# Performance work log

Measured on AMD Instinct MI355X. Metric: run time of the kernel, lower is better.

## Reference

```python
import jax, jax.numpy as jnp
import numpy as np


def setup_inputs() -> dict:
    key = jax.random.key(0)
    ks = jax.random.split(key, 8)
    N, DIN, DOUT = 8192, 1024, 1024
    s = 1.0 / np.sqrt(DIN)
    return {
        "gAB": jax.random.normal(ks[0], (N, DIN), dtype=jnp.float32),
        "gAG": jax.random.normal(ks[1], (N, DIN), dtype=jnp.float32),
        "Wab": jax.random.normal(ks[2], (DIN, DOUT), dtype=jnp.float32) * s,
        "Wag": jax.random.normal(ks[3], (DIN, DOUT), dtype=jnp.float32) * s,
        "bab": jax.random.normal(ks[4], (DOUT,), dtype=jnp.float32) * 0.01,
        "bag": jax.random.normal(ks[5], (DOUT,), dtype=jnp.float32) * 0.01,
        "sAB": jax.random.normal(ks[6], (N, DOUT), dtype=jnp.float32),
        "sAG": jax.random.normal(ks[7], (N, DOUT), dtype=jnp.float32),
    }


def reference(gAB, gAG, Wab, Wag, bab, bag, sAB, sAG) -> jnp.ndarray:
    # project() per encoder (Linear): [N, DIN] @ [DIN, DOUT] + b
    pAB = gAB @ Wab + bab  # [N, DOUT]
    pAG = gAG @ Wag + bag  # [N, DOUT]
    # torch.diag(pAB @ pAG.T) == row-wise dot product (avoids O(N^2 d) waste)
    h1 = jnp.sum(pAB * pAG, axis=1, keepdims=True)  # [N, 1]
    h2 = jnp.sum(sAB * sAG, axis=1, keepdims=True)  # [N, 1]
    # mean over concatenated (h1, h2) columns, keepdim=True
    h = jnp.mean(jnp.concatenate([h1, h2], axis=1), axis=1, keepdims=True)  # [N, 1]
    return h
```

## Files before the change

### kernel.cpp

```cpp
#include <hip/hip_runtime.h>
#include <hip/hip_bf16.h>
#include <stdint.h>

typedef __attribute__((ext_vector_type(8))) short bf16x8;
typedef __attribute__((ext_vector_type(4))) float f32x4;

#define DIN 1024
#define NROWS 8192

__device__ __forceinline__ unsigned short f2bf(float f) {
    union { float f; unsigned u; } v; v.f = f;
    unsigned r = v.u + 0x7FFFu + ((v.u >> 16) & 1u);
    return (unsigned short)(r >> 16);
}

__device__ __forceinline__ int fswz(int r) { return (r ^ (r >> 2)) & 3; }

__device__ __forceinline__ size_t swz8_byte(int R, int c) {
    return ((size_t)R * DIN + (size_t)(c & ~63)) * 2
         + (size_t)(((((c >> 3) & 7) ^ (R & 7)) << 4))
         + (size_t)((c & 7) * 2);
}

__device__ __forceinline__ void gload_lds16(const void* g, void* l) {
    __builtin_amdgcn_global_load_lds(
        (const __attribute__((address_space(1))) unsigned*)g,
        (__attribute__((address_space(3))) unsigned*)l, 16, 0, 0);
}

__global__ __launch_bounds__(256) void prep_kernel(const float* __restrict__ Wab,
                                                   const float* __restrict__ Wag,
                                                   const float* __restrict__ bab,
                                                   const float* __restrict__ bag,
                                                   float* __restrict__ ws_f,
                                                   unsigned short* __restrict__ Whab,
                                                   unsigned short* __restrict__ Whag) {
    int b = blockIdx.x;
    int wave = threadIdx.x >> 6, lane = threadIdx.x & 63;
    if (b == 256) {
        if (wave == 0) {
            float acc = 0.f;
            for (int j = lane; j < DIN; j += 64) acc += bab[j] * bag[j];
            for (int off = 32; off; off >>= 1) acc += __shfl_xor(acc, off);
            if (lane == 0) ws_f[2048] = acc;
        }
        return;
    }
    int r = b * 4 + wave;
    int fr = fswz(r);
    {
        const float* wrow = Wab + (size_t)r * DIN;
        char* hrow = (char*)Whab + (size_t)r * DIN * 2;
        float acc = 0.f;
#pragma unroll
        for (int it = 0; it < 4; ++it) {
            int col = it * 256 + lane * 4;
            float4 w = *reinterpret_cast<const float4*>(wrow + col);
            float4 bv = *reinterpret_cast<const float4*>(bag + col);
            acc += w.x * bv.x + w.y * bv.y + w.z * bv.z + w.w * bv.w;
            ushort4 h; h.x = f2bf(w.x); h.y = f2bf(w.y); h.z = f2bf(w.z); h.w = f2bf(w.w);
            *reinterpret_cast<ushort4*>(hrow + (col & ~31) * 2 + ((((col >> 3) & 3) ^ fr) << 4) + (col & 7) * 2) = h;
        }
        for (int off = 32; off; off >>= 1) acc += __shfl_xor(acc, off);
        if (lane == 0) ws_f[r] = acc;
    }
    {
        const float* wrow = Wag + (size_t)r * DIN;
        char* hrow = (char*)Whag + (size_t)r * DIN * 2;
        float acc = 0.f;
#pragma unroll
        for (int it = 0; it < 4; ++it) {
            int col = it * 256 + lane * 4;
            float4 w = *reinterpret_cast<const float4*>(wrow + col);
            float4 bv = *reinterpret_cast<const float4*>(bab + col);
            acc += w.x * bv.x + w.y * bv.y + w.z * bv.z + w.w * bv.w;
            ushort4 h; h.x = f2bf(w.x); h.y = f2bf(w.y); h.z = f2bf(w.z); h.w = f2bf(w.w);
            *reinterpret_cast<ushort4*>(hrow + (col & ~31) * 2 + ((((col >> 3) & 3) ^ fr) << 4) + (col & 7) * 2) = h;
        }
        for (int off = 32; off; off >>= 1) acc += __shfl_xor(acc, off);
        if (lane == 0) ws_f[1024 + r] = acc;
    }
}

__global__ __launch_bounds__(512) void mt_kernel(const unsigned short* __restrict__ Whag,
                                                 const unsigned short* __restrict__ Whab,
                                                 unsigned short* __restrict__ Mt) {
    __shared__ unsigned short sm[2][2][2][2048];
    int tid = threadIdx.x;
    int wave = tid >> 6, grp = wave >> 2, w4 = wave & 3;
    int lane = tid & 63, kg = lane >> 4, cl = lane & 15;
    int wr = w4 >> 1, wc = w4 & 1;
    int br = blockIdx.x >> 4, bc = blockIdx.x & 15;
    int u = tid & 255, urow = u >> 2, uchunk = u & 3;

    const char* Abase = (const char*)Whag + ((size_t)(br * 64 + urow) * DIN + grp * 512) * 2 + uchunk * 16;
    const char* Bbase = (const char*)Whab + ((size_t)(bc * 64 + urow) * DIN + grp * 512) * 2 + uchunk * 16;

    int offA[2], offB[2];
#pragma unroll
    for (int m = 0; m < 2; ++m) { int row = wr * 32 + m * 16 + cl; offA[m] = row * 32 + ((kg ^ fswz(row)) << 3); }
#pragma unroll
    for (int n = 0; n < 2; ++n) { int row = wc * 32 + n * 16 + cl; offB[n] = row * 32 + ((kg ^ fswz(row)) << 3); }

    f32x4 acc[2][2] = {};
    gload_lds16(Abase, &sm[grp][0][0][u * 8]);
    gload_lds16(Bbase, &sm[grp][0][1][u * 8]);
    for (int t = 0; t < 16; ++t) {
        int p = t & 1;
        __syncthreads();
        if (t < 15) {
            gload_lds16(Abase + (t + 1) * 64, &sm[grp][p ^ 1][0][u * 8]);
            gload_lds16(Bbase + (t + 1) * 64, &sm[grp][p ^ 1][1][u * 8]);
        }
        bf16x8 af[2], bfr[2];
#pragma unroll
        for (int m = 0; m < 2; ++m) af[m] = *reinterpret_cast<const bf16x8*>(&sm[grp][p][0][offA[m]]);
#pragma unroll
        for (int n = 0; n < 2; ++n) bfr[n] = *reinterpret_cast<const bf16x8*>(&sm[grp][p][1][offB[n]]);
        __builtin_amdgcn_s_setprio(1);
#pragma unroll
        for (int m = 0; m < 2; ++m)
#pragma unroll
            for (int n = 0; n < 2; ++n)
                acc[m][n] = __builtin_amdgcn_mfma_f32_16x16x32_bf16(af[m], bfr[n], acc[m][n], 0, 0, 0);
        __builtin_amdgcn_s_setprio(0);
    }
    __syncthreads();
    float* red = (float*)sm;
    if (grp == 1) {
#pragma unroll
        for (int m = 0; m < 2; ++m)
#pragma unroll
            for (int n = 0; n < 2; ++n)
#pragma unroll
                for (int j = 0; j < 4; ++j)
                    red[(wr * 32 + m * 16 + kg * 4 + j) * 68 + wc * 32 + n * 16 + cl] = acc[m][n][j];
    }
    __syncthreads();
    if (grp == 0) {
#pragma unroll
        for (int m = 0; m < 2; ++m)
#pragma unroll
            for (int n = 0; n < 2; ++n)
#pragma unroll
                for (int j = 0; j < 4; ++j) {
                    int rl = wr * 32 + m * 16 + kg * 4 + j, cll = wc * 32 + n * 16 + cl;
                    float v = acc[m][n][j] + red[rl * 68 + cll];
                    int R = br * 64 + rl, C = bc * 64 + cll;
                    *(unsigned short*)((char*)Mt + swz8_byte(R, C)) = f2bf(v);
                }
    }
}

__global__ __launch_bounds__(256) void stream_kernel(const float* __restrict__ gAB,
                                                     const float* __restrict__ sAB,
                                                     const float* __restrict__ sAG,
                                                     const float* __restrict__ ws_f,
                                                     unsigned short* __restrict__ gABh,
                                                     float* __restrict__ out,
                                                     int writecast) {
    int wave = threadIdx.x >> 6, lane = threadIdx.x & 63;
    int row = blockIdx.x * 4 + wave;
    const float* ga = gAB + (size_t)row * DIN;
    const float* sa = sAB + (size_t)row * DIN;
    const float* sg = sAG + (size_t)row * DIN;
    char* gh = (char*)gABh + (size_t)row * DIN * 2;
    int fr8 = row & 7;
    float acc = 0.f;
#pragma unroll
    for (int cc = 0; cc < 4; ++cc) {
        int col = cc * 256 + lane * 4;
        float4 a = *reinterpret_cast<const float4*>(ga + col);
        float4 x = *reinterpret_cast<const float4*>(sa + col);
        float4 y = *reinterpret_cast<const float4*>(sg + col);
        float4 v = *reinterpret_cast<const float4*>(ws_f + col);
        acc += x.x * y.x + x.y * y.y + x.z * y.z + x.w * y.w;
        acc += a.x * v.x + a.y * v.y + a.z * v.z + a.w * v.w;
        if (writecast) {
            ushort4 h; h.x = f2bf(a.x); h.y = f2bf(a.y); h.z = f2bf(a.z); h.w = f2bf(a.w);
            *reinterpret_cast<ushort4*>(gh + (col & ~63) * 2 + ((((col >> 3) & 7) ^ fr8) << 4) + (col & 7) * 2) = h;
        }
    }
#pragma unroll
    for (int off = 32; off; off >>= 1) acc += __shfl_xor(acc, off);
    if (lane == 0) out[row] = 0.5f * (acc + ws_f[2048]);
}

template <int PRECAST>
__global__ __launch_bounds__(512, 2) void gemm256(const float* __restrict__ gAB,
                                                  const unsigned short* __restrict__ gABh,
                                                  const float* __restrict__ gAG,
                                                  const unsigned short* __restrict__ Mt,
                                                  const float* __restrict__ ws_f,
                                                  float* __restrict__ out) {
    __shared__ unsigned short lds_a[2][256 * 64];
    __shared__ unsigned short lds_b[2][256 * 64];
    constexpr int KSPLIT = 2, KLEN = DIN / KSPLIT, NSTEP = KLEN / 64;
    int b = blockIdx.x;
    int x = b & 7, s = b >> 3;
    int rblk = x + 8 * (s & 3);
    int rem = s >> 2;
    int ks = rem & 1;
    int cblk = rem >> 1;
    int tid = threadIdx.x, wave = tid >> 6, lane = tid & 63;
    int wr = wave >> 2, wc = wave & 3;
    int kg = lane >> 4, cl = lane & 15;
    int row0 = rblk * 256, col0 = cblk * 256;

    const char* Ab = (const char*)gABh + (size_t)row0 * DIN * 2 + (size_t)(ks * KLEN) * 2;
    const char* Bb = (const char*)Mt + (size_t)col0 * DIN * 2 + (size_t)(ks * KLEN) * 2;
    const float* Af = gAB + (size_t)row0 * DIN + ks * KLEN;

    f32x4 acc[8][4] = {};

#define STAGE_B(buf, t)                                                                   \
    _Pragma("unroll")                                                                     \
    for (int it = 0; it < 4; ++it) {                                                      \
        int u = tid + it * 512;                                                           \
        gload_lds16(Bb + (size_t)(u >> 3) * (DIN * 2) + (u & 7) * 16 + (t) * 128,         \
                    (char*)&lds_b[buf][0] + u * 16);                                      \
    }
#define STAGE_A_PRE(buf, t)                                                               \
    _Pragma("unroll")                                                                     \
    for (int it = 0; it < 4; ++it) {                                                      \
        int u = tid + it * 512;                                                           \
        gload_lds16(Ab + (size_t)(u >> 3) * (DIN * 2) + (u & 7) * 16 + (t) * 128,         \
                    (char*)&lds_a[buf][0] + u * 16);                                      \
    }
#define STAGE_A_F32(buf, t)                                                               \
    _Pragma("unroll")                                                                     \
    for (int it = 0; it < 8; ++it) {                                                      \
        int u = tid + it * 512;                                              \
        int row = u >> 4, c4 = u & 15;                          \
        float4 w = *reinterpret_cast<const float4*>(Af + (size_t)row * DIN + (t) * 64 + c4 * 4); \
        ushort4 h; h.x = f2bf(w.x); h.y = f2bf(w.y); h.z = f2bf(w.z); h.w = f2bf(w.w);    \
        *reinterpret_cast<ushort4*>((char*)&lds_a[buf][0] + row * 128 +                   \
                                    (((c4 >> 1) ^ (row & 7)) << 4) + (c4 & 1) * 8) = h;   \
    }

    if (PRECAST) { STAGE_A_PRE(0, 0); } else { STAGE_A_F32(0, 0); }
    STAGE_B(0, 0);

    for (int t = 0; t < NSTEP; ++t) {
        int p = t & 1;
        __syncthreads();
        if (t < NSTEP - 1) {
            if (PRECAST) { STAGE_A_PRE(p ^ 1, t + 1); } else { STAGE_A_F32(p ^ 1, t + 1); }
            STAGE_B(p ^ 1, t + 1);
        }
#pragma unroll
        for (int kk = 0; kk < 2; ++kk) {
            bf16x8 bfr[4];
#pragma unroll
            for (int n = 0; n < 4; ++n) {
                int row = wc * 64 + n * 16 + cl;
                bfr[n] = *reinterpret_cast<const bf16x8*>(&lds_b[p][row * 64 + ((((kk << 2) | kg) ^ (row & 7)) << 3)]);
            }
            bf16x8 af[8];
#pragma unroll
            for (int m = 0; m < 8; ++m) {
                int row = wr * 128 + m * 16 + cl;
                af[m] = *reinterpret_cast<const bf16x8*>(&lds_a[p][row * 64 + ((((kk << 2) | kg) ^ (row & 7)) << 3)]);
            }
            __builtin_amdgcn_s_setprio(1);
#pragma unroll
            for (int m = 0; m < 8; ++m)
#pragma unroll
                for (int n = 0; n < 4; ++n)
                    acc[m][n] = __builtin_amdgcn_mfma_f32_16x16x32_bf16(af[m], bfr[n], acc[m][n], 0, 0, 0);
            __builtin_amdgcn_s_setprio(0);
        }
    }

    const float* vag = ws_f + 1024;
#pragma unroll
    for (int m = 0; m < 8; ++m)
#pragma unroll
        for (int j = 0; j < 4; ++j) {
            int row = row0 + wr * 128 + m * 16 + kg * 4 + j;
            const float* gr = gAG + (size_t)row * DIN;
            float t = 0.f;
#pragma unroll
            for (int n = 0; n < 4; ++n) {
                int col = col0 + wc * 64 + n * 16 + cl;
                float addv = (ks == 0) ? vag[col] : 0.f;
                t += gr[col] * (acc[m][n][j] + addv);
            }
            t += __shfl_xor(t, 1);
            t += __shfl_xor(t, 2);
            t += __shfl_xor(t, 4);
            t += __shfl_xor(t, 8);
            if (cl == 0) atomicAdd(out + row, 0.5f * t);
        }
#undef STAGE_B
#undef STAGE_A_PRE
#undef STAGE_A_F32
}

extern "C" void kernel_launch(void* const* d_in, const int* in_sizes, int n_in,
                              void* d_out, int out_size, void* d_ws, size_t ws_size,
                              hipStream_t stream) {
    const float* gAB = (const float*)d_in[0];
    const float* gAG = (const float*)d_in[1];
    const float* Wab = (const float*)d_in[2];
    const float* Wag = (const float*)d_in[3];
    const float* bab = (const float*)d_in[4];
    const float* bag = (const float*)d_in[5];
    const float* sAB = (const float*)d_in[6];
    const float* sAG = (const float*)d_in[7];
    float* out = (float*)d_out;

    float* ws_f = (float*)d_ws;
    char* base = (char*)d_ws + 16384;
    unsigned short* Mt = (unsigned short*)base;
    unsigned short* Whag = (unsigned short*)(base + (size_t)2 * 1024 * 1024);
    unsigned short* Whab = (unsigned short*)(base + (size_t)4 * 1024 * 1024);
    unsigned short* gABh = (unsigned short*)(base + (size_t)6 * 1024 * 1024);
    size_t need_full = 16384 + (size_t)22 * 1024 * 1024;
    int precast = (ws_size >= need_full) ? 1 : 0;

    prep_kernel<<<257, 256, 0, stream>>>(Wab, Wag, bab, bag, ws_f, Whab, Whag);
    mt_kernel<<<256, 512, 0, stream>>>(Whag, Whab, Mt);
    stream_kernel<<<2048, 256, 0, stream>>>(gAB, sAB, sAG, ws_f, gABh, out, precast);
    if (precast)
        gemm256<1><<<256, 512, 0, stream>>>(gAB, gABh, gAG, Mt, ws_f, out);
    else
        gemm256<0><<<256, 512, 0, stream>>>(gAB, gABh, gAG, Mt, ws_f, out);
}
```

Measured before the change: 71.64 us.

## Triple-buffer GEMM with BK=32 stages and explicit vmcnt waits, add fallback GEMM

Replaces the double-buffered 256x256 GEMM (K-step 64) with a three-stage pipeline using K-step 32 tiles. Loads are issued two steps ahead, and a single barrier per step is guarded by explicit s_waitcnt vmcnt counts instead of __syncthreads. LDS swizzle offsets are precomputed once per thread. The non-precast path gets a separate 128x128 kernel with register-staged fp32 loads. The aim is to hide global-to-LDS latency better. In exchange it halves MFMA work per barrier and lowers the occupancy hint to one block per CU.

New measurement: 78.01 us. +8.9%, slower.

```diff
diff --git a/kernel.cpp b/kernel.cpp
--- a/kernel.cpp
+++ b/kernel.cpp
@@ -186,16 +186,14 @@
     if (lane == 0) out[row] = 0.5f * (acc + ws_f[2048]);
 }
 
-template <int PRECAST>
-__global__ __launch_bounds__(512, 2) void gemm256(const float* __restrict__ gAB,
-                                                  const unsigned short* __restrict__ gABh,
-                                                  const float* __restrict__ gAG,
-                                                  const unsigned short* __restrict__ Mt,
-                                                  const float* __restrict__ ws_f,
-                                                  float* __restrict__ out) {
-    __shared__ unsigned short lds_a[2][256 * 64];
-    __shared__ unsigned short lds_b[2][256 * 64];
-    constexpr int KSPLIT = 2, KLEN = DIN / KSPLIT, NSTEP = KLEN / 64;
+__global__ __launch_bounds__(512, 1) void gemm_pipe(const unsigned short* __restrict__ gABh,
+                                                    const float* __restrict__ gAG,
+                                                    const unsigned short* __restrict__ Mt,
+                                                    const float* __restrict__ ws_f,
+                                                    float* __restrict__ out) {
+    __shared__ unsigned short lds_a[3][256 * 32];
+    __shared__ unsigned short lds_b[3][256 * 32];
+    constexpr int KLEN = 512, NSTEP = 16;
     int b = blockIdx.x;
     int x = b & 7, s = b >> 3;
     int rblk = x + 8 * (s & 3);
@@ -207,70 +205,71 @@
     int kg = lane >> 4, cl = lane & 15;
     int row0 = rblk * 256, col0 = cblk * 256;
 
-    const char* Ab = (const char*)gABh + (size_t)row0 * DIN * 2 + (size_t)(ks * KLEN) * 2;
-    const char* Bb = (const char*)Mt + (size_t)col0 * DIN * 2 + (size_t)(ks * KLEN) * 2;
-    const float* Af = gAB + (size_t)row0 * DIN + ks * KLEN;
+    const char* Ab = (const char*)gABh + (size_t)row0 * (DIN * 2) + (size_t)ks * KLEN * 2;
+    const char* Bb = (const char*)Mt + (size_t)col0 * (DIN * 2) + (size_t)ks * KLEN * 2;
+
+    int offA[8], offB[4];
+#pragma unroll
+    for (int m = 0; m < 8; ++m) { int row = wr * 128 + m * 16 + cl; offA[m] = row * 64 + ((kg ^ (row & 3)) << 4); }
+#pragma unroll
+    for (int n = 0; n < 4; ++n) { int row = wc * 64 + n * 16 + cl; offB[n] = row * 64 + ((kg ^ (row & 3)) << 4); }
+
+#define STAGE(buf, t) do {                                                          \
+    _Pragma("unroll")                                                               \
+    for (int it = 0; it < 2; ++it) {                                                \
+        int u = tid + it * 512;                                                     \
+        int row_ = u >> 2, s_ = u & 3;                                              \
+        int pg = ((((t) & 1) << 2) ^ (row_ & 4)) | s_;                              \
+        gload_lds16(Ab + (size_t)row_ * 2048 + ((t) >> 1) * 128 + pg * 16,          \
+                    (char*)&lds_a[buf][0] + u * 16);                                \
+    }                                                                               \
+    _Pragma("unroll")                                                               \
+    for (int it = 0; it < 2; ++it) {                                                \
+        int u = tid + it * 512;                                                     \
+        int row_ = u >> 2, s_ = u & 3;                                              \
+        int pg = ((((t) & 1) << 2) ^ (row_ & 4)) | s_;                              \
+        gload_lds16(Bb + (size_t)row_ * 2048 + ((t) >> 1) * 128 + pg * 16,          \
+                    (char*)&lds_b[buf][0] + u * 16);                                \
+    }                                                                               \
+} while (0)
 
     f32x4 acc[8][4] = {};
 
-#define STAGE_B(buf, t)                                                                   \
-    _Pragma("unroll")                                                                     \
-    for (int it = 0; it < 4; ++it) {                                                      \
-        int u = tid + it * 512;                                                           \
-        gload_lds16(Bb + (size_t)(u >> 3) * (DIN * 2) + (u & 7) * 16 + (t) * 128,         \
-                    (char*)&lds_b[buf][0] + u * 16);                                      \
-    }
-#define STAGE_A_PRE(buf, t)                                                               \
-    _Pragma("unroll")                                                                     \
-    for (int it = 0; it < 4; ++it) {                                                      \
-        int u = tid + it * 512;                                                           \
-        gload_lds16(Ab + (size_t)(u >> 3) * (DIN * 2) + (u & 7) * 16 + (t) * 128,         \
-                    (char*)&lds_a[buf][0] + u * 16);                                      \
-    }
-#define STAGE_A_F32(buf, t)                                                               \
-    _Pragma("unroll")                                                                     \
-    for (int it = 0; it < 8; ++it) {                                                      \
-        int u = tid + it * 512;                                              \
-        int row = u >> 4, c4 = u & 15;                          \
-        float4 w = *reinterpret_cast<const float4*>(Af + (size_t)row * DIN + (t) * 64 + c4 * 4); \
-        ushort4 h; h.x = f2bf(w.x); h.y = f2bf(w.y); h.z = f2bf(w.z); h.w = f2bf(w.w);    \
-        *reinterpret_cast<ushort4*>((char*)&lds_a[buf][0] + row * 128 +                   \
-                                    (((c4 >> 1) ^ (row & 7)) << 4) + (c4 & 1) * 8) = h;   \
-    }
-
-    if (PRECAST) { STAGE_A_PRE(0, 0); } else { STAGE_A_F32(0, 0); }
-    STAGE_B(0, 0);
+    STAGE(0, 0);
+    STAGE(1, 1);
+    asm volatile("s_waitcnt vmcnt(4)" ::: "memory");
+    __builtin_amdgcn_sched_barrier(0);
+    __builtin_amdgcn_s_barrier();
+    __builtin_amdgcn_sched_barrier(0);
 
     for (int t = 0; t < NSTEP; ++t) {
-        int p = t & 1;
-        __syncthreads();
-        if (t < NSTEP - 1) {
-            if (PRECAST) { STAGE_A_PRE(p ^ 1, t + 1); } else { STAGE_A_F32(p ^ 1, t + 1); }
-            STAGE_B(p ^ 1, t + 1);
-        }
-#pragma unroll
-        for (int kk = 0; kk < 2; ++kk) {
-            bf16x8 bfr[4];
-#pragma unroll
-            for (int n = 0; n < 4; ++n) {
-                int row = wc * 64 + n * 16 + cl;
-                bfr[n] = *reinterpret_cast<const bf16x8*>(&lds_b[p][row * 64 + ((((kk << 2) | kg) ^ (row & 7)) << 3)]);
-            }
-            bf16x8 af[8];
-#pragma unroll
-            for (int m = 0; m < 8; ++m) {
-                int row = wr * 128 + m * 16 + cl;
-                af[m] = *reinterpret_cast<const bf16x8*>(&lds_a[p][row * 64 + ((((kk << 2) | kg) ^ (row & 7)) << 3)]);
-            }
-            __builtin_amdgcn_s_setprio(1);
-#pragma unroll
-            for (int m = 0; m < 8; ++m)
-#pragma unroll
-                for (int n = 0; n < 4; ++n)
-                    acc[m][n] = __builtin_amdgcn_mfma_f32_16x16x32_bf16(af[m], bfr[n], acc[m][n], 0, 0, 0);
-            __builtin_amdgcn_s_setprio(0);
-        }
-    }
+        int cur = t % 3;
+        if (t < NSTEP - 2) {
+            int nxt = (t + 2) % 3;
+            STAGE(nxt, t + 2);
+        }
+        bf16x8 af[8], bfr[4];
+#pragma unroll
+        for (int n = 0; n < 4; ++n) bfr[n] = *reinterpret_cast<const bf16x8*>((char*)&lds_b[cur][0] + offB[n]);
+#pragma unroll
+        for (int m = 0; m < 8; ++m) af[m] = *reinterpret_cast<const bf16x8*>((char*)&lds_a[cur][0] + offA[m]);
+        __builtin_amdgcn_s_setprio(1);
+#pragma unroll
+        for (int m = 0; m < 8; ++m)
+#pragma unroll
+            for (int n = 0; n < 4; ++n)
+                acc[m][n] = __builtin_amdgcn_mfma_f32_16x16x32_bf16(af[m], bfr[n], acc[m][n], 0, 0, 0);
+        __builtin_amdgcn_s_setprio(0);
+        if (t < NSTEP - 2) {
+            asm volatile("s_waitcnt vmcnt(4)" ::: "memory");
+        } else {
+            asm volatile("s_waitcnt vmcnt(0)" ::: "memory");
+        }
+        __builtin_amdgcn_sched_barrier(0);
+        __builtin_amdgcn_s_barrier();
+        __builtin_amdgcn_sched_barrier(0);
+    }
+#undef STAGE
 
     const float* vag = ws_f + 1024;
 #pragma unroll
@@ -292,9 +291,99 @@
             t += __shfl_xor(t, 8);
             if (cl == 0) atomicAdd(out + row, 0.5f * t);
         }
-#undef STAGE_B
-#undef STAGE_A_PRE
-#undef STAGE_A_F32
+}
+
+__global__ __launch_bounds__(256, 4) void gemm_fb(const float* __restrict__ gAB,
+                                                  const float* __restrict__ gAG,
+                                                  const unsigned short* __restrict__ Mt,
+                                                  const float* __restrict__ ws_f,
+                                                  float* __restrict__ out) {
+    __shared__ unsigned short lds_a[2][128 * 32];
+    __shared__ unsigned short lds_b[2][128 * 32];
+    constexpr int KSPLIT = 2, KLEN = DIN / KSPLIT, NSTEP = KLEN / 32;
+    int b = blockIdx.x;
+    int x = b & 7, s = b >> 3;
+    int rblk = x + 8 * (s & 7);
+    int u2 = s >> 3;
+    int ks = u2 & (KSPLIT - 1);
+    int cblk = u2 / KSPLIT;
+    int tid = threadIdx.x, wave = tid >> 6, lane = tid & 63;
+    int wr = wave >> 1, wc = wave & 1;
+    int kg = lane >> 4, cl = lane & 15;
+    int row0 = rblk * 128, col0 = cblk * 128;
+
+    int offA[4], offB[4];
+#pragma unroll
+    for (int m = 0; m < 4; ++m) { int row = wr * 64 + m * 16 + cl; offA[m] = row * 64 + ((kg ^ (row & 3)) << 4); }
+#pragma unroll
+    for (int n = 0; n < 4; ++n) { int row = wc * 64 + n * 16 + cl; offB[n] = row * 64 + ((kg ^ (row & 3)) << 4); }
+
+    const float* Af = gAB + (size_t)row0 * DIN + ks * KLEN;
+    const char* Bb = (const char*)Mt + ((size_t)col0 * DIN + ks * KLEN) * 2;
+
+    f32x4 acc[4][4] = {};
+    float4 ra[4];
+#define STAGE_A(buf, t)                                                             \
+    _Pragma("unroll")                                                               \
+    for (int it = 0; it < 4; ++it) {                                                \
+        int u = tid + it * 256, row_ = u >> 3, c4 = u & 7;                          \
+        ra[it] = *reinterpret_cast<const float4*>(Af + (size_t)row_ * DIN + (t) * 32 + c4 * 4); \
+    }                                                                               \
+    _Pragma("unroll")                                                               \
+    for (int it = 0; it < 4; ++it) {                                                \
+        int u = tid + it * 256, row_ = u >> 3, c4 = u & 7;                          \
+        ushort4 h; h.x = f2bf(ra[it].x); h.y = f2bf(ra[it].y); h.z = f2bf(ra[it].z); h.w = f2bf(ra[it].w); \
+        *reinterpret_cast<ushort4*>((char*)&lds_a[buf][0] + row_ * 64 +             \
+                                    (((c4 >> 1) ^ (row_ & 3)) << 4) + (c4 & 1) * 8) = h; \
+    }
+#define STAGE_Bm(buf, t)                                                            \
+    _Pragma("unroll")                                                               \
+    for (int it = 0; it < 2; ++it) {                                                \
+        int u = tid + it * 256, row_ = u >> 2, s_ = u & 3;                          \
+        int pg = ((((t) & 1) << 2) ^ (row_ & 4)) | s_;                              \
+        gload_lds16(Bb + (size_t)row_ * 2048 + ((t) >> 1) * 128 + pg * 16,          \
+                    (char*)&lds_b[buf][0] + u * 16);                                \
+    }
+    STAGE_A(0, 0);
+    STAGE_Bm(0, 0);
+    for (int t = 0; t < NSTEP; ++t) {
+        int p = t & 1;
+        __syncthreads();
+        if (t < NSTEP - 1) { STAGE_Bm(p ^ 1, t + 1); }
+        bf16x8 af[4], bfr[4];
+#pragma unroll
+        for (int m = 0; m < 4; ++m) af[m] = *reinterpret_cast<const bf16x8*>((char*)&lds_a[p][0] + offA[m]);
+#pragma unroll
+        for (int n = 0; n < 4; ++n) bfr[n] = *reinterpret_cast<const bf16x8*>((char*)&lds_b[p][0] + offB[n]);
+#pragma unroll
+        for (int m = 0; m < 4; ++m)
+#pragma unroll
+            for (int n = 0; n < 4; ++n)
+                acc[m][n] = __builtin_amdgcn_mfma_f32_16x16x32_bf16(af[m], bfr[n], acc[m][n], 0, 0, 0);
+        if (t < NSTEP - 1) { STAGE_A(p ^ 1, t + 1); }
+    }
+#undef STAGE_A
+#undef STAGE_Bm
+    const float* vag = ws_f + 1024;
+#pragma unroll
+    for (int m = 0; m < 4; ++m)
+#pragma unroll
+        for (int j = 0; j < 4; ++j) {
+            int row = row0 + wr * 64 + m * 16 + kg * 4 + j;
+            const float* gr = gAG + (size_t)row * DIN;
+            float t = 0.f;
+#pragma unroll
+            for (int n = 0; n < 4; ++n) {
+                int col = col0 + wc * 64 + n * 16 + cl;
+                float addv = (ks == 0) ? vag[col] : 0.f;
+                t += gr[col] * (acc[m][n][j] + addv);
+            }
+            t += __shfl_xor(t, 1);
+            t += __shfl_xor(t, 2);
+            t += __shfl_xor(t, 4);
+            t += __shfl_xor(t, 8);
+            if (cl == 0) atomicAdd(out + row, 0.5f * t);
+        }
 }
 
 extern "C" void kernel_launch(void* const* d_in, const int* in_sizes, int n_in,
@@ -323,7 +412,7 @@
     mt_kernel<<<256, 512, 0, stream>>>(Whag, Whab, Mt);
     stream_kernel<<<2048, 256, 0, stream>>>(gAB, sAB, sAG, ws_f, gABh, out, precast);
     if (precast)
-        gemm256<1><<<256, 512, 0, stream>>>(gAB, gABh, gAG, Mt, ws_f, out);
+        gemm_pipe<<<256, 512, 0, stream>>>(gABh, gAG, Mt, ws_f, out);
     else
-        gemm256<0><<<256, 512, 0, stream>>>(gAB, gABh, gAG, Mt, ws_f, out);
-}
+        gemm_fb<<<1024, 256, 0, stream>>>(gAB, gAG, Mt, ws_f, out);
+}
```
